# Performance work log

Hardware: AMD Instinct MI355X
Metric: run time of the kernel (lower is better)

Reference implementation:

```python
import jax, jax.numpy as jnp
import numpy as np

B, C, H, W = 8, 512, 64, 64
NH, D = 8, 64            # num_heads, head_dim (C = NH*D)
WH, WW = 8, 8            # window size
EPS = 1e-5
SCALE = D ** -0.5


def _layernorm(x, g, b):
    mu = jnp.mean(x, axis=-1, keepdims=True)
    var = jnp.mean((x - mu) ** 2, axis=-1, keepdims=True)
    return (x - mu) * jax.lax.rsqrt(var + EPS) * g + b


def _rope_cache(n, d):
    pos = jnp.arange(n, dtype=jnp.float32)
    inv_freq = 1.0 / (10000.0 ** (jnp.arange(0, d, 2, dtype=jnp.float32) / d))
    sinusoid = pos[:, None] * inv_freq[None, :]          # (n, d//2)
    return jnp.stack([jnp.sin(sinusoid), jnp.cos(sinusoid)], axis=-1).reshape(n, d)


def _apply_rope(x, rope):
    # x: (B, nH, N, d); rope: (N, d) packed [sin, cos] interleaved
    b, nh, n, d = x.shape
    x_ = x.reshape(b, nh, n, d // 2, 2)
    r = rope.reshape(n, d // 2, 2)
    sin, cos = r[..., 0], r[..., 1]                      # (N, d//2)
    x0, x1 = x_[..., 0], x_[..., 1]
    xr0 = x0 * cos - x1 * sin
    xr1 = x0 * sin + x1 * cos
    return jnp.stack([xr0, xr1], axis=-1).reshape(b, nh, n, d)


def _relative_index(wh, ww):
    ch, cw = np.meshgrid(np.arange(wh), np.arange(ww), indexing='ij')
    flat = np.stack([ch.reshape(-1), cw.reshape(-1)])    # (2, Ws)
    rel = flat[:, :, None] - flat[:, None, :]            # (2, Ws, Ws)
    rel = rel.transpose(1, 2, 0).astype(np.int64)
    rel[..., 0] += wh - 1
    rel[..., 1] += ww - 1
    rel[..., 0] *= 2 * ww - 1
    return jnp.asarray(rel.sum(-1))                      # (Ws, Ws)


def setup_inputs() -> dict:
    key = jax.random.key(0)
    ks = jax.random.split(key, 12)
    s = 0.02
    table_size = (2 * WH - 1) * (2 * WW - 1)
    return {
        'q':  jax.random.normal(ks[0], (B, C, H, W), jnp.float32),
        'kv': jax.random.normal(ks[1], (B, C, H, W), jnp.float32),
        'g_q':  jnp.ones((C,), jnp.float32),  'b_q_ln':  jnp.zeros((C,), jnp.float32),
        'g_kv': jnp.ones((C,), jnp.float32),  'b_kv_ln': jnp.zeros((C,), jnp.float32),
        'Wq': jax.random.normal(ks[2], (C, C), jnp.float32) * s, 'bq': jnp.zeros((C,), jnp.float32),
        'Wk': jax.random.normal(ks[3], (C, C), jnp.float32) * s, 'bk': jnp.zeros((C,), jnp.float32),
        'Wv': jax.random.normal(ks[4], (C, C), jnp.float32) * s, 'bv': jnp.zeros((C,), jnp.float32),
        'Wo': jax.random.normal(ks[5], (C, C), jnp.float32) * s, 'bo': jnp.zeros((C,), jnp.float32),
        'bias_table': jax.random.normal(ks[6], (table_size, NH), jnp.float32) * s,
    }


def reference(q, kv, g_q, b_q_ln, g_kv, b_kv_ln, Wq, bq, Wk, bk, Wv, bv, Wo, bo, bias_table):
    N = H * W
    Hn, Wn = H // WH, W // WW
    nw = Hn * Wn
    Ws = WH * WW

    # flatten NCHW -> (B, N, C)
    q_seq = q.reshape(B, C, N).transpose(0, 2, 1)
    kv_seq = kv.reshape(B, C, N).transpose(0, 2, 1)
    q_seq = _layernorm(q_seq, g_q, b_q_ln)
    kv_seq = _layernorm(kv_seq, g_kv, b_kv_ln)

    Q = (q_seq @ Wq.T + bq).reshape(B, N, NH, D).transpose(0, 2, 1, 3)   # (B,nH,N,d)
    K = (kv_seq @ Wk.T + bk).reshape(B, N, NH, D).transpose(0, 2, 1, 3)
    V = (kv_seq @ Wv.T + bv).reshape(B, N, NH, D).transpose(0, 2, 1, 3)

    rope = _rope_cache(N, D)
    Q = _apply_rope(Q, rope)
    K = _apply_rope(K, rope)

    # window partition: (B,nH,H,W,d) -> (nH, B*nw, Ws, d); head-major to match torch cat order
    def part(x):
        x = x.reshape(B, NH, Hn, WH, Wn, WW, D)
        return x.transpose(1, 0, 2, 4, 3, 5, 6).reshape(NH, B * nw, Ws, D)

    Qw, Kw, Vw = part(Q), part(K), part(V)

    attn = jnp.einsum('hnqd,hnkd->hnqk', Qw, Kw) * SCALE                 # (nH, B*nw, Ws, Ws)
    rel_idx = _relative_index(WH, WW)
    bias = bias_table[rel_idx.reshape(-1)].reshape(Ws, Ws, NH).transpose(2, 0, 1)  # (nH, Ws, Ws)
    attn = attn + bias[:, None, :, :]
    attn = jax.nn.softmax(attn, axis=-1)
    out_w = jnp.einsum('hnqk,hnkd->hnqd', attn, Vw)                      # (nH, B*nw, Ws, d)

    # window reverse + head concat -> (B, N, C)
    out = out_w.reshape(NH, B, Hn, Wn, WH, WW, D)
    out = out.transpose(1, 2, 4, 3, 5, 0, 6).reshape(B, N, NH * D)

    out = out @ Wo.T + bo
    out = out + q_seq                                                    # residual w/ normed q (as in source)
    return out.transpose(0, 2, 1).reshape(B, C, H, W)
```

## Files before the change

### kernel.cpp

```cpp
#include <hip/hip_runtime.h>


typedef unsigned short u16;
typedef __bf16 bf16x8 __attribute__((ext_vector_type(8)));
typedef float f32x4 __attribute__((ext_vector_type(4)));
typedef u16 u16x8 __attribute__((ext_vector_type(8)));
typedef u16 u16x4 __attribute__((ext_vector_type(4)));

__device__ __forceinline__ u16 f2bf(float f) {
    __bf16 h = (__bf16)f;
    return __builtin_bit_cast(u16, h);
}
__device__ __forceinline__ float bf2f(u16 u) {
    return (float)__builtin_bit_cast(__bf16, u);
}
__device__ __forceinline__ f32x4 mfma16(bf16x8 a, bf16x8 b, f32x4 c) {
    return __builtin_amdgcn_mfma_f32_16x16x32_bf16(a, b, c, 0, 0, 0);
}
__device__ __forceinline__ void gl_lds16(const u16* g, u16* l) {
    __builtin_amdgcn_global_load_lds((const __attribute__((address_space(1))) void*)g,
                                     (__attribute__((address_space(3))) void*)l, 16, 0, 0);
}
__device__ __forceinline__ int swapb(int n) {
    return (n & 0xE07) | ((n & 0x1C0) >> 3) | ((n & 0x038) << 3);
}

__global__ __launch_bounds__(256) void setup_kernel(
    const float* __restrict__ Wq, const float* __restrict__ Wk,
    const float* __restrict__ Wv, const float* __restrict__ Wo,
    const float* __restrict__ btab,
    u16* __restrict__ wq, u16* __restrict__ wk,
    u16* __restrict__ wv, u16* __restrict__ wo,
    float* __restrict__ rope, float* __restrict__ biasf)
{
    int idx = blockIdx.x * 256 + threadIdx.x;
    {
        int w = idx >> 18, e = idx & 262143;
        const float* src = (w == 0) ? Wq : (w == 1) ? Wk : (w == 2) ? Wv : Wo;
        u16* dst = (w == 0) ? wq : (w == 1) ? wk : (w == 2) ? wv : wo;
        dst[e] = f2bf(src[e]);
    }
    if (idx < 131072) {
        int n = idx >> 5, j = idx & 31;
        float inv = powf(10000.0f, -(float)j / 32.0f);
        float a = (float)n * inv;
        float s, c;
        sincosf(a, &s, &c);
        rope[n * 64 + 2 * j] = s;
        rope[n * 64 + 2 * j + 1] = c;
    }
    if (idx < 32768) {
        int q = idx & 63, pp = (idx >> 6) & 63, h = idx >> 12;
        int r1 = pp >> 3, c1 = pp & 7, r2 = q >> 3, c2 = q & 7;
        int ri = (r1 - r2 + 7) * 15 + (c1 - c2 + 7);
        biasf[idx] = btab[ri * 8 + h];
    }
}

__global__ __launch_bounds__(256) void ln_kernel(
    const float* __restrict__ x, const float* __restrict__ g,
    const float* __restrict__ be, u16* __restrict__ out)
{
    __shared__ u16 sX[512 * 36];
    __shared__ float sS[1024];
    __shared__ float sQ[1024];
    __shared__ float sMu[32], sInv[32];

    const int tid = threadIdx.x;
    const int b = blockIdx.x >> 7, grp = blockIdx.x & 127;
    const int nbase = grp << 5;
    const int t4 = tid & 7;
    const int cg = tid >> 3;

    const float* xp = x + ((size_t)b << 21) + nbase + (t4 << 2);
    float sm[4] = {0.f, 0.f, 0.f, 0.f}, sq2[4] = {0.f, 0.f, 0.f, 0.f};
#pragma unroll 4
    for (int it = 0; it < 16; it++) {
        int c = (it << 5) + cg;
        f32x4 v = *(const f32x4*)&xp[(size_t)c << 12];
        u16x4 h;
#pragma unroll
        for (int r = 0; r < 4; r++) {
            sm[r] += v[r];
            sq2[r] += v[r] * v[r];
            h[r] = f2bf(v[r]);
        }
        *(u16x4*)&sX[c * 36 + (t4 << 2)] = h;
    }
#pragma unroll
    for (int r = 0; r < 4; r++) {
        sS[tid * 4 + r] = sm[r];
        sQ[tid * 4 + r] = sq2[r];
    }
    __syncthreads();
    if (tid < 32) {
        int t4v = tid >> 2, r = tid & 3;
        float a = 0.f, q2 = 0.f;
#pragma unroll
        for (int c2 = 0; c2 < 32; c2++) {
            int i2 = ((c2 << 3) + t4v) * 4 + r;
            a += sS[i2];
            q2 += sQ[i2];
        }
        float mu = a * (1.f / 512.f);
        float var = q2 * (1.f / 512.f) - mu * mu;
        sMu[tid] = mu;
        sInv[tid] = rsqrtf(var + 1e-5f);
    }
    __syncthreads();

    const int t = tid >> 3;
    const int cs = (tid & 7) << 3;
    float mu = sMu[t], inv = sInv[t];
    int p = swapb(nbase + t);
    size_t orow = ((size_t)((b << 12) + p)) * 512;
#pragma unroll
    for (int it = 0; it < 8; it++) {
        int c0 = cs + (it << 6);
        f32x4 g0 = *(const f32x4*)&g[c0];
        f32x4 g1 = *(const f32x4*)&g[c0 + 4];
        f32x4 e0 = *(const f32x4*)&be[c0];
        f32x4 e1 = *(const f32x4*)&be[c0 + 4];
        u16x8 o;
#pragma unroll
        for (int k = 0; k < 8; k++) {
            float v = bf2f(sX[(c0 + k) * 36 + t]);
            float gg = (k < 4) ? g0[k] : g1[k - 4];
            float bb = (k < 4) ? e0[k] : e1[k - 4];
            o[k] = f2bf((v - mu) * inv * gg + bb);
        }
        *(u16x8*)&out[orow + c0] = o;
    }
}

__global__ __launch_bounds__(512, 2) void gemm_qkv(
    const u16* __restrict__ qn, const u16* __restrict__ kvn,
    const u16* __restrict__ wq, const u16* __restrict__ wk, const u16* __restrict__ wv,
    const float* __restrict__ bq, const float* __restrict__ bk, const float* __restrict__ bv,
    const float* __restrict__ rope,
    u16* __restrict__ Qr, u16* __restrict__ Kr, u16* __restrict__ VT)
{
    __shared__ __align__(16) u16 smem[65536];

    const int bid = blockIdx.x;
    const int swz = (bid & 7) * 96 + (bid >> 3);
    const int kind = swz >> 8;
    const int rem = swz & 255;
    const int n0 = (rem >> 7) << 8;
    const int m0 = (rem & 127) << 8;

    const u16* Asrc = (kind == 0) ? qn : kvn;
    const u16* W = (kind == 0) ? wq : (kind == 1) ? wk : wv;
    const float* bias = (kind == 0) ? bq : (kind == 1) ? bk : bv;

    const int tid = threadIdx.x;
    const int lane = tid & 63, wid = tid >> 6;
    const int ln = lane & 15, lq = lane >> 4;
    const int wr = wid >> 2, wc = wid & 3;

    const int rr = tid >> 2;
    const int cc = (tid & 3) ^ ((tid >> 3) & 3);
    const u16* aSt = Asrc + (size_t)(m0 + rr) * 512 + cc * 8;
    const u16* bSt = W + (size_t)(n0 + rr) * 512 + cc * 8;
    const int aD = wid * 512;

#pragma unroll
    for (int t = 0; t < 4; ++t) {
        const u16* ga = aSt + t * 32;
        const u16* gb = bSt + t * 32;
        gl_lds16(ga, &smem[(t << 13) + aD]);
        gl_lds16(ga + (size_t)(128 * 512), &smem[(t << 13) + 4096 + aD]);
        gl_lds16(gb, &smem[32768 + (t << 13) + aD]);
        gl_lds16(gb + (size_t)(128 * 512), &smem[32768 + (t << 13) + 4096 + aD]);
    }

    const int swzc = lq ^ ((ln >> 1) & 3);
    const int aRd = (wr * 128 + ln) * 32 + swzc * 8;
    const int bRd = (wc * 64 + ln) * 32 + swzc * 8;

    f32x4 acc[8][4] = {};

    asm volatile("s_waitcnt vmcnt(12)" ::: "memory");
    __builtin_amdgcn_s_barrier();
    __builtin_amdgcn_sched_barrier(0);

    for (int kt = 0; kt < 16; ++kt) {
        const int sAo = (kt & 3) << 13;
        const int sBo = 32768 + sAo;
        f32x4 a0 = *(const f32x4*)&smem[sAo + aRd];
        f32x4 a1 = *(const f32x4*)&smem[sAo + aRd + 512];
        f32x4 a2 = *(const f32x4*)&smem[sAo + aRd + 1024];
        f32x4 a3 = *(const f32x4*)&smem[sAo + aRd + 1536];
        f32x4 b0 = *(const f32x4*)&smem[sBo + bRd];
        f32x4 b1 = *(const f32x4*)&smem[sBo + bRd + 512];
        f32x4 b2 = *(const f32x4*)&smem[sBo + bRd + 1024];
        f32x4 b3 = *(const f32x4*)&smem[sBo + bRd + 1536];
        asm volatile("" ::"v"(a0), "v"(a1), "v"(a2), "v"(a3),
                         "v"(b0), "v"(b1), "v"(b2), "v"(b3));
        __builtin_amdgcn_s_barrier();
        __builtin_amdgcn_sched_barrier(0);
        if (kt < 12) {
            const u16* gb = bSt + (size_t)(kt + 4) * 32;
            gl_lds16(gb, &smem[sBo + aD]);
            gl_lds16(gb + (size_t)(128 * 512), &smem[sBo + 4096 + aD]);
        }
        f32x4 h0 = *(const f32x4*)&smem[sAo + aRd + 2048];
        f32x4 h1 = *(const f32x4*)&smem[sAo + aRd + 2560];
        f32x4 h2 = *(const f32x4*)&smem[sAo + aRd + 3072];
        f32x4 h3 = *(const f32x4*)&smem[sAo + aRd + 3584];
        __builtin_amdgcn_sched_barrier(0);
        {
            bf16x8 bA[4] = {__builtin_bit_cast(bf16x8, a0), __builtin_bit_cast(bf16x8, a1),
                            __builtin_bit_cast(bf16x8, a2), __builtin_bit_cast(bf16x8, a3)};
            bf16x8 bB[4] = {__builtin_bit_cast(bf16x8, b0), __builtin_bit_cast(bf16x8, b1),
                            __builtin_bit_cast(bf16x8, b2), __builtin_bit_cast(bf16x8, b3)};
            __builtin_amdgcn_s_setprio(1);
#pragma unroll
            for (int i = 0; i < 4; ++i)
#pragma unroll
                for (int j = 0; j < 4; ++j)
                    acc[i][j] = mfma16(bA[i], bB[j], acc[i][j]);
            __builtin_amdgcn_s_setprio(0);
            asm volatile("" ::"v"(h0), "v"(h1), "v"(h2), "v"(h3));
            __builtin_amdgcn_s_barrier();
            __builtin_amdgcn_sched_barrier(0);
            if (kt < 12) {
                const u16* ga = aSt + (size_t)(kt + 4) * 32;
                gl_lds16(ga, &smem[sAo + aD]);
                gl_lds16(ga + (size_t)(128 * 512), &smem[sAo + 4096 + aD]);
            }
            bf16x8 hA[4] = {__builtin_bit_cast(bf16x8, h0), __builtin_bit_cast(bf16x8, h1),
                            __builtin_bit_cast(bf16x8, h2), __builtin_bit_cast(bf16x8, h3)};
            __builtin_amdgcn_s_setprio(1);
#pragma unroll
            for (int i = 0; i < 4; ++i)
#pragma unroll
                for (int j = 0; j < 4; ++j)
                    acc[i + 4][j] = mfma16(hA[i], bB[j], acc[i + 4][j]);
            __builtin_amdgcn_s_setprio(0);
        }
        if (kt < 12) {
            asm volatile("s_waitcnt vmcnt(12)" ::: "memory");
        } else if (kt == 12) {
            asm volatile("s_waitcnt vmcnt(8)" ::: "memory");
        } else if (kt == 13) {
            asm volatile("s_waitcnt vmcnt(4)" ::: "memory");
        } else if (kt == 14) {
            asm volatile("s_waitcnt vmcnt(0)" ::: "memory");
        }
        if (kt < 15) {
            __builtin_amdgcn_s_barrier();
            __builtin_amdgcn_sched_barrier(0);
        }
    }

    float bj[4];
#pragma unroll
    for (int j = 0; j < 4; ++j) bj[j] = bias[n0 + wc * 64 + j * 16 + ln];

    u16* sU = smem;

    if (kind < 2) {
        u16* Out = (kind == 0) ? Qr : Kr;
#pragma unroll
        for (int g = 0; g < 4; ++g) {
            __syncthreads();
            if (wr == (g >> 1)) {
                const int i0 = (g & 1) * 4;
#pragma unroll
                for (int di = 0; di < 4; ++di)
#pragma unroll
                    for (int j = 0; j < 4; ++j)
#pragma unroll
                        for (int r = 0; r < 4; ++r)
                            sU[(di * 16 + lq * 4 + r) * 264 + wc * 64 + j * 16 + ln] =
                                f2bf(acc[i0 + di][j][r] + bj[j]);
            }
            __syncthreads();
#pragma unroll
            for (int it = 0; it < 4; ++it) {
                int idx = it * 512 + tid;
                int row = idx >> 5;
                int cseg = (idx & 31) << 3;
                u16x8 v = *(const u16x8*)&sU[row * 264 + cseg];
                int t = m0 + g * 64 + row;
                int n = swapb(t & 4095);
                float f[8];
#pragma unroll
                for (int k = 0; k < 8; k++) f[k] = bf2f(v[k]);
                {
                    int d0 = cseg & 63;
                    const float* rp = &rope[n * 64 + d0];
                    f32x4 r0 = *(const f32x4*)rp;
                    f32x4 r1 = *(const f32x4*)(rp + 4);
#pragma unroll
                    for (int pp = 0; pp < 4; pp++) {
                        float sn = (pp < 2) ? r0[2 * pp] : r1[2 * (pp - 2)];
                        float cs2 = (pp < 2) ? r0[2 * pp + 1] : r1[2 * (pp - 2) + 1];
                        float x0 = f[2 * pp], x1 = f[2 * pp + 1];
                        f[2 * pp] = x0 * cs2 - x1 * sn;
                        f[2 * pp + 1] = x0 * sn + x1 * cs2;
                    }
                }
                u16x8 o;
#pragma unroll
                for (int k = 0; k < 8; k++) o[k] = f2bf(f[k]);
                *(u16x8*)&Out[(size_t)t * 512 + n0 + cseg] = o;
            }
        }
    } else {
        const int wq0 = m0 & 4095;
        const int bb = m0 >> 12;
#pragma unroll
        for (int g = 0; g < 4; ++g) {
            __syncthreads();
            if (wc == g) {
#pragma unroll
                for (int i = 0; i < 8; ++i)
#pragma unroll
                    for (int j = 0; j < 4; ++j) {
                        u16x4 pk;
#pragma unroll
                        for (int r = 0; r < 4; ++r) pk[r] = f2bf(acc[i][j][r] + bj[j]);
                        *(u16x4*)&sU[(j * 16 + ln) * 264 + wr * 128 + i * 16 + lq * 4] = pk;
                    }
            }
            __syncthreads();
#pragma unroll
            for (int it = 0; it < 4; ++it) {
                int idx = it * 512 + tid;
                int col = idx >> 5;
                int ch = (idx & 31) << 3;
                u16x8 v = *(const u16x8*)&sU[col * 264 + ch];
                int c = n0 + g * 64 + col;
                int hh = c >> 6, dd = c & 63;
                *(u16x8*)&VT[((size_t)((((bb << 3) + hh) << 6) + dd)) * 4096 + wq0 + ch] = v;
            }
        }
    }
}

__global__ __launch_bounds__(256) void gemm_out(
    const u16* __restrict__ A, const u16* __restrict__ Bw,
    const float* __restrict__ bias, const u16* __restrict__ qn,
    float* __restrict__ Out)
{
    __shared__ u16 sA[128 * 32];
    __shared__ u16 sB[128 * 32];
    __shared__ u16 sR[128 * 136];

    const int m0 = blockIdx.x * 128;
    const int n0 = blockIdx.y * 128;
    const int tid = threadIdx.x;
    const int lane = tid & 63, wave = tid >> 6;
    const int ln = lane & 15, lq = lane >> 4;
    const int wm = wave & 1, wn = wave >> 1;

    const int srow = wave * 16 + (lane >> 2);
    const int sseg = (lane & 3) << 3;
    const u16* gA0 = A + (size_t)(m0 + srow) * 512 + sseg;
    const u16* gA1 = gA0 + (size_t)64 * 512;
    const u16* gB0 = Bw + (size_t)(n0 + srow) * 512 + sseg;
    const u16* gB1 = gB0 + (size_t)64 * 512;
    u16* lA0 = &sA[wave * 16 * 32];
    u16* lA1 = &sA[(64 + wave * 16) * 32];
    u16* lB0 = &sB[wave * 16 * 32];
    u16* lB1 = &sB[(64 + wave * 16) * 32];

    f32x4 acc[4][4] = {};

    for (int kt = 0; kt < 512; kt += 32) {
        gl_lds16(gA0 + kt, lA0);
        gl_lds16(gA1 + kt, lA1);
        gl_lds16(gB0 + kt, lB0);
        gl_lds16(gB1 + kt, lB1);
        __syncthreads();
        bf16x8 af[4], bfr[4];
#pragma unroll
        for (int i = 0; i < 4; i++)
            af[i] = *(const bf16x8*)&sA[(wm * 64 + i * 16 + ln) * 32 + lq * 8];
#pragma unroll
        for (int j = 0; j < 4; j++)
            bfr[j] = *(const bf16x8*)&sB[(wn * 64 + j * 16 + ln) * 32 + lq * 8];
#pragma unroll
        for (int i = 0; i < 4; i++)
#pragma unroll
            for (int j = 0; j < 4; j++)
                acc[i][j] = mfma16(af[i], bfr[j], acc[i][j]);
        __syncthreads();
    }

#pragma unroll
    for (int it = 0; it < 8; it++) {
        int idx = it * 256 + tid;
        int row = idx >> 4, c8 = (idx & 15) << 3;
        *(u16x8*)&sR[row * 136 + c8] = *(const u16x8*)&qn[(size_t)(m0 + row) * 512 + n0 + c8];
    }
    __syncthreads();

    int cj[4];
    float bj[4];
#pragma unroll
    for (int j = 0; j < 4; j++) {
        cj[j] = n0 + wn * 64 + j * 16 + ln;
        bj[j] = bias[cj[j]];
    }
#pragma unroll
    for (int i = 0; i < 4; i++) {
        int t0 = m0 + wm * 64 + i * 16 + lq * 4;
        int bb = t0 >> 12;
        int nb = swapb(t0 & 4095);
        int lrow = wm * 64 + i * 16 + lq * 4;
#pragma unroll
        for (int j = 0; j < 4; j++) {
            int lcol = wn * 64 + j * 16 + ln;
            f32x4 v;
#pragma unroll
            for (int r = 0; r < 4; r++)
                v[r] = acc[i][j][r] + bj[j] + bf2f(sR[(lrow + r) * 136 + lcol]);
            *(f32x4*)&Out[((size_t)((bb << 9) + cj[j]) << 12) + nb] = v;
        }
    }
}

__global__ __launch_bounds__(256) void attn_kernel(
    const u16* __restrict__ Q, const u16* __restrict__ K, const u16* __restrict__ VT,
    const float* __restrict__ biasf, u16* __restrict__ Out)
{
    __shared__ u16 sQ[64 * 72];
    __shared__ u16 sK[64 * 72];
    __shared__ u16 sVT[64 * 72];
    __shared__ u16 sP[4][16 * 72];

    const int tid = threadIdx.x;
    const int h = blockIdx.x & 7;
    const int w = (blockIdx.x >> 3) & 63;
    const int b = blockIdx.x >> 9;
    const int lane = tid & 63, wave = tid >> 6;
    const int ln = lane & 15, lq = lane >> 4;

    const size_t qrow0 = (size_t)(b << 12) + w * 64;
    const size_t vrow0 = ((size_t)(((b << 3) + h) << 6)) * 4096 + w * 64;

#pragma unroll
    for (int ii = 0; ii < 2; ii++) {
        int idx = ii * 256 + tid;
        int row = idx >> 3, ch = (idx & 7) << 3;
        size_t ga = (qrow0 + row) * 512 + h * 64 + ch;
        *(u16x8*)&sQ[row * 72 + ch] = *(const u16x8*)&Q[ga];
        *(u16x8*)&sK[row * 72 + ch] = *(const u16x8*)&K[ga];
        *(u16x8*)&sVT[row * 72 + ch] = *(const u16x8*)&VT[vrow0 + (size_t)row * 4096 + ch];
    }
    __syncthreads();

    f32x4 s[4] = {};
#pragma unroll
    for (int ks = 0; ks < 2; ks++) {
        bf16x8 a = *(const bf16x8*)&sQ[(wave * 16 + ln) * 72 + ks * 32 + lq * 8];
#pragma unroll
        for (int j = 0; j < 4; j++) {
            bf16x8 bb = *(const bf16x8*)&sK[(j * 16 + ln) * 72 + ks * 32 + lq * 8];
            s[j] = mfma16(a, bb, s[j]);
        }
    }

    float sv[4][4];
#pragma unroll
    for (int r = 0; r < 4; r++) {
        const float* bp = &biasf[((h * 64 + wave * 16 + lq * 4 + r) << 6) + ln];
#pragma unroll
        for (int j = 0; j < 4; j++) sv[r][j] = s[j][r] * 0.125f + bp[j * 16];
    }
#pragma unroll
    for (int r = 0; r < 4; r++) {
        float m = fmaxf(fmaxf(sv[r][0], sv[r][1]), fmaxf(sv[r][2], sv[r][3]));
        m = fmaxf(m, __shfl_xor(m, 1));
        m = fmaxf(m, __shfl_xor(m, 2));
        m = fmaxf(m, __shfl_xor(m, 4));
        m = fmaxf(m, __shfl_xor(m, 8));
        float sum = 0.f;
#pragma unroll
        for (int j = 0; j < 4; j++) {
            sv[r][j] = __expf(sv[r][j] - m);
            sum += sv[r][j];
        }
        sum += __shfl_xor(sum, 1);
        sum += __shfl_xor(sum, 2);
        sum += __shfl_xor(sum, 4);
        sum += __shfl_xor(sum, 8);
        float rinv = 1.f / sum;
#pragma unroll
        for (int j = 0; j < 4; j++)
            sP[wave][(lq * 4 + r) * 72 + j * 16 + ln] = f2bf(sv[r][j] * rinv);
    }

    f32x4 o[4] = {};
#pragma unroll
    for (int ks = 0; ks < 2; ks++) {
        bf16x8 a = *(const bf16x8*)&sP[wave][ln * 72 + ks * 32 + lq * 8];
#pragma unroll
        for (int jd = 0; jd < 4; jd++) {
            bf16x8 bb = *(const bf16x8*)&sVT[(jd * 16 + ln) * 72 + ks * 32 + lq * 8];
            o[jd] = mfma16(a, bb, o[jd]);
        }
    }

#pragma unroll
    for (int r = 0; r < 4; r++)
#pragma unroll
        for (int jd = 0; jd < 4; jd++)
            sQ[(wave * 16 + lq * 4 + r) * 72 + jd * 16 + ln] = f2bf(o[jd][r]);
    __syncthreads();
#pragma unroll
    for (int ii = 0; ii < 2; ii++) {
        int idx = ii * 256 + tid;
        int row = idx >> 3, ch = (idx & 7) << 3;
        *(u16x8*)&Out[(qrow0 + row) * 512 + h * 64 + ch] = *(const u16x8*)&sQ[row * 72 + ch];
    }
}

extern "C" void kernel_launch(void* const* d_in, const int* in_sizes, int n_in,
                              void* d_out, int out_size, void* d_ws, size_t ws_size,
                              hipStream_t stream)
{
    const float* q    = (const float*)d_in[0];
    const float* kv   = (const float*)d_in[1];
    const float* g_q  = (const float*)d_in[2];
    const float* b_q  = (const float*)d_in[3];
    const float* g_kv = (const float*)d_in[4];
    const float* b_kv = (const float*)d_in[5];
    const float* Wq   = (const float*)d_in[6];
    const float* bq   = (const float*)d_in[7];
    const float* Wk   = (const float*)d_in[8];
    const float* bk   = (const float*)d_in[9];
    const float* Wv   = (const float*)d_in[10];
    const float* bv   = (const float*)d_in[11];
    const float* Wo   = (const float*)d_in[12];
    const float* bo   = (const float*)d_in[13];
    const float* btab = (const float*)d_in[14];

    char* ws = (char*)d_ws;
    u16* qn      = (u16*)(ws);
    u16* kvn     = (u16*)(ws + 33554432);
    u16* VT      = (u16*)(ws + 67108864);
    float* rope  = (float*)(ws + 100663296);
    float* biasf = (float*)(ws + 101711872);
    u16* wq      = (u16*)(ws + 101842944);
    u16* wk      = (u16*)(ws + 102367232);
    u16* wv      = (u16*)(ws + 102891520);
    u16* wo      = (u16*)(ws + 103415808);
    u16* aout    = kvn;
    u16* Qr      = (u16*)d_out;
    u16* Kr      = Qr + 16777216;

    setup_kernel<<<4096, 256, 0, stream>>>(Wq, Wk, Wv, Wo, btab, wq, wk, wv, wo, rope, biasf);
    ln_kernel<<<1024, 256, 0, stream>>>(q, g_q, b_q, qn);
    ln_kernel<<<1024, 256, 0, stream>>>(kv, g_kv, b_kv, kvn);
    gemm_qkv<<<768, 512, 0, stream>>>(qn, kvn, wq, wk, wv, bq, bk, bv, rope, Qr, Kr, VT);
    attn_kernel<<<4096, 256, 0, stream>>>(Qr, Kr, VT, biasf, aout);
    gemm_out<<<dim3(256, 4), 256, 0, stream>>>(aout, wo, bo, qn, (float*)d_out);
}
```

Before: 349.0 us.

## Restructure QKV GEMM main loop to a 3-deep prefetch with one barrier

The 4-stage LDS ring is now filled with a 3-tile prefetch distance. All global-to-LDS loads for tile kt+3 are issued at the top of each iteration instead of being split between two barriers inside it. The per-iteration barriers and scheduling fences that were interleaved with the LDS reads are removed and the k-loop is fully unrolled, letting the compiler schedule LDS reads and MFMAs freely. The aim is less barrier stall per iteration. The cost is a shorter prefetch lead and less explicit control over instruction ordering.

```diff
diff --git a/kernel.cpp b/kernel.cpp
--- a/kernel.cpp
+++ b/kernel.cpp
@@ -165,13 +165,13 @@
     const int aD = wid * 512;
 
 #pragma unroll
-    for (int t = 0; t < 4; ++t) {
+    for (int t = 0; t < 3; ++t) {
         const u16* ga = aSt + t * 32;
         const u16* gb = bSt + t * 32;
-        gl_lds16(ga, &smem[(t << 13) + aD]);
-        gl_lds16(ga + (size_t)(128 * 512), &smem[(t << 13) + 4096 + aD]);
-        gl_lds16(gb, &smem[32768 + (t << 13) + aD]);
-        gl_lds16(gb + (size_t)(128 * 512), &smem[32768 + (t << 13) + 4096 + aD]);
+        gl_lds16(ga, &smem[t * 8192 + aD]);
+        gl_lds16(ga + (size_t)(128 * 512), &smem[t * 8192 + 4096 + aD]);
+        gl_lds16(gb, &smem[32768 + t * 8192 + aD]);
+        gl_lds16(gb + (size_t)(128 * 512), &smem[32768 + t * 8192 + 4096 + aD]);
     }
 
     const int swzc = lq ^ ((ln >> 1) & 3);
@@ -180,68 +180,46 @@
 
     f32x4 acc[8][4] = {};
 
-    asm volatile("s_waitcnt vmcnt(12)" ::: "memory");
+    asm volatile("s_waitcnt vmcnt(8)" ::: "memory");
     __builtin_amdgcn_s_barrier();
     __builtin_amdgcn_sched_barrier(0);
 
+#pragma unroll
     for (int kt = 0; kt < 16; ++kt) {
-        const int sAo = (kt & 3) << 13;
+        const int sAo = (kt & 3) * 8192;
         const int sBo = 32768 + sAo;
-        f32x4 a0 = *(const f32x4*)&smem[sAo + aRd];
-        f32x4 a1 = *(const f32x4*)&smem[sAo + aRd + 512];
-        f32x4 a2 = *(const f32x4*)&smem[sAo + aRd + 1024];
-        f32x4 a3 = *(const f32x4*)&smem[sAo + aRd + 1536];
-        f32x4 b0 = *(const f32x4*)&smem[sBo + bRd];
-        f32x4 b1 = *(const f32x4*)&smem[sBo + bRd + 512];
-        f32x4 b2 = *(const f32x4*)&smem[sBo + bRd + 1024];
-        f32x4 b3 = *(const f32x4*)&smem[sBo + bRd + 1536];
-        asm volatile("" ::"v"(a0), "v"(a1), "v"(a2), "v"(a3),
-                         "v"(b0), "v"(b1), "v"(b2), "v"(b3));
-        __builtin_amdgcn_s_barrier();
-        __builtin_amdgcn_sched_barrier(0);
-        if (kt < 12) {
-            const u16* gb = bSt + (size_t)(kt + 4) * 32;
-            gl_lds16(gb, &smem[sBo + aD]);
-            gl_lds16(gb + (size_t)(128 * 512), &smem[sBo + 4096 + aD]);
-        }
-        f32x4 h0 = *(const f32x4*)&smem[sAo + aRd + 2048];
-        f32x4 h1 = *(const f32x4*)&smem[sAo + aRd + 2560];
-        f32x4 h2 = *(const f32x4*)&smem[sAo + aRd + 3072];
-        f32x4 h3 = *(const f32x4*)&smem[sAo + aRd + 3584];
-        __builtin_amdgcn_sched_barrier(0);
-        {
-            bf16x8 bA[4] = {__builtin_bit_cast(bf16x8, a0), __builtin_bit_cast(bf16x8, a1),
-                            __builtin_bit_cast(bf16x8, a2), __builtin_bit_cast(bf16x8, a3)};
-            bf16x8 bB[4] = {__builtin_bit_cast(bf16x8, b0), __builtin_bit_cast(bf16x8, b1),
-                            __builtin_bit_cast(bf16x8, b2), __builtin_bit_cast(bf16x8, b3)};
-            __builtin_amdgcn_s_setprio(1);
-#pragma unroll
-            for (int i = 0; i < 4; ++i)
-#pragma unroll
-                for (int j = 0; j < 4; ++j)
-                    acc[i][j] = mfma16(bA[i], bB[j], acc[i][j]);
-            __builtin_amdgcn_s_setprio(0);
-            asm volatile("" ::"v"(h0), "v"(h1), "v"(h2), "v"(h3));
-            __builtin_amdgcn_s_barrier();
-            __builtin_amdgcn_sched_barrier(0);
-            if (kt < 12) {
-                const u16* ga = aSt + (size_t)(kt + 4) * 32;
-                gl_lds16(ga, &smem[sAo + aD]);
-                gl_lds16(ga + (size_t)(128 * 512), &smem[sAo + 4096 + aD]);
-            }
-            bf16x8 hA[4] = {__builtin_bit_cast(bf16x8, h0), __builtin_bit_cast(bf16x8, h1),
-                            __builtin_bit_cast(bf16x8, h2), __builtin_bit_cast(bf16x8, h3)};
-            __builtin_amdgcn_s_setprio(1);
-#pragma unroll
-            for (int i = 0; i < 4; ++i)
-#pragma unroll
-                for (int j = 0; j < 4; ++j)
-                    acc[i + 4][j] = mfma16(hA[i], bB[j], acc[i + 4][j]);
-            __builtin_amdgcn_s_setprio(0);
-        }
-        if (kt < 12) {
-            asm volatile("s_waitcnt vmcnt(12)" ::: "memory");
-        } else if (kt == 12) {
+        if (kt <= 12) {
+            const u16* ga = aSt + (size_t)(kt + 3) * 32;
+            const u16* gb = bSt + (size_t)(kt + 3) * 32;
+            const int d = ((kt + 3) & 3) * 8192;
+            gl_lds16(ga, &smem[d + aD]);
+            gl_lds16(ga + (size_t)(128 * 512), &smem[d + 4096 + aD]);
+            gl_lds16(gb, &smem[32768 + d + aD]);
+            gl_lds16(gb + (size_t)(128 * 512), &smem[32768 + d + 4096 + aD]);
+        }
+        bf16x8 A0[4], A1[4], Bf[4];
+#pragma unroll
+        for (int i = 0; i < 4; ++i)
+            A0[i] = *(const bf16x8*)&smem[sAo + aRd + i * 512];
+#pragma unroll
+        for (int j = 0; j < 4; ++j)
+            Bf[j] = *(const bf16x8*)&smem[sBo + bRd + j * 512];
+#pragma unroll
+        for (int i = 0; i < 4; ++i)
+            A1[i] = *(const bf16x8*)&smem[sAo + aRd + 2048 + i * 512];
+        __builtin_amdgcn_s_setprio(1);
+#pragma unroll
+        for (int i = 0; i < 4; ++i)
+#pragma unroll
+            for (int j = 0; j < 4; ++j)
+                acc[i][j] = mfma16(A0[i], Bf[j], acc[i][j]);
+#pragma unroll
+        for (int i = 0; i < 4; ++i)
+#pragma unroll
+            for (int j = 0; j < 4; ++j)
+                acc[i + 4][j] = mfma16(A1[i], Bf[j], acc[i + 4][j]);
+        __builtin_amdgcn_s_setprio(0);
+        if (kt < 13) {
             asm volatile("s_waitcnt vmcnt(8)" ::: "memory");
         } else if (kt == 13) {
             asm volatile("s_waitcnt vmcnt(4)" ::: "memory");
```

New measurement: 346.7 us. No clear change (-0.7%).
